# Optimization experiments

Hardware: AMD Instinct MI355X
Metric: run time of the kernel (lower is better)

Reference implementation:

```python
import jax, jax.numpy as jnp
import numpy as np

B, S, D, H = 4, 2048, 1024, 16
HD = D // H


def setup_inputs() -> dict:
    key = jax.random.key(0)
    ks = jax.random.split(key, 10)
    x = jax.random.normal(ks[0], (B, S, D), dtype=jnp.float32)
    mask = jnp.zeros((B, 1, 1, S), dtype=jnp.float32)  # 1 = masked, 0 = keep
    sc = 1.0 / np.sqrt(D)
    wq = jax.random.normal(ks[1], (D, D), dtype=jnp.float32) * sc
    wk = jax.random.normal(ks[2], (D, D), dtype=jnp.float32) * sc
    wv = jax.random.normal(ks[3], (D, D), dtype=jnp.float32) * sc
    wo = jax.random.normal(ks[4], (D, D), dtype=jnp.float32) * sc
    bq = jnp.zeros((D,), jnp.float32)
    bk = jnp.zeros((D,), jnp.float32)
    bv = jnp.zeros((D,), jnp.float32)
    bo = jnp.zeros((D,), jnp.float32)
    return {"x": x, "mask": mask, "wq": wq, "bq": bq, "wk": wk, "bk": bk,
            "wv": wv, "bv": bv, "wo": wo, "bo": bo}


def _split_heads(t):
    # (B, S, D) -> (B, H, S, HD)
    return t.reshape(B, -1, H, HD).transpose(0, 2, 1, 3)


def reference(x, mask, wq, bq, wk, bk, wv, bv, wo, bo):
    q = _split_heads(x @ wq + bq)
    k = _split_heads(x @ wk + bk)
    v = _split_heads(x @ wv + bv)
    # scaled dot-product attention (TF tutorial convention: mask*-1e9 added)
    scores = jnp.einsum("bhqd,bhkd->bhqk", q, k) / jnp.sqrt(jnp.float32(HD))
    scores = scores + mask * -1e9
    attn_weights = jax.nn.softmax(scores, axis=-1)  # (B, H, Sq, Sk)
    attn = jnp.einsum("bhqk,bhkd->bhqd", attn_weights, v)
    attn = attn.transpose(0, 2, 1, 3).reshape(B, -1, D)
    out = attn @ wo + bo
    return out, attn_weights
```

## Files before the change

### kernel.cpp

```cpp
#include <hip/hip_runtime.h>
#include <hip/hip_bf16.h>

#define S_LEN  2048
#define DMODEL 1024
#define NHEAD  16
#define HDIM   64
#define BSZ    4

#define C_SCORE  0.18033688f
#define C_MASK  -1.4426950e9f

typedef __bf16 bf16_t;
typedef __bf16 bf16x8 __attribute__((ext_vector_type(8)));
typedef __bf16 bf16x4 __attribute__((ext_vector_type(4)));
typedef float  f32x4  __attribute__((ext_vector_type(4)));

typedef __attribute__((address_space(1))) void as1_void;
typedef __attribute__((address_space(3))) void as3_void;

__device__ __forceinline__ f32x4 mfma16(bf16x8 a, bf16x8 b, f32x4 c) {
    return __builtin_amdgcn_mfma_f32_16x16x32_bf16(a, b, c, 0, 0, 0);
}

__global__ __launch_bounds__(256) void cvt_all(const float* __restrict__ x,
                                               bf16_t* __restrict__ xb,
                                               const float* __restrict__ w0,
                                               const float* __restrict__ w1,
                                               const float* __restrict__ w2,
                                               const float* __restrict__ w3,
                                               bf16_t* __restrict__ wT) {
    __shared__ bf16_t t[64][65];
    const int bid = blockIdx.x;
    if (bid < 4096) {
        const int i0 = bid * 256 + threadIdx.x;
        #pragma unroll
        for (int rep = 0; rep < 2; ++rep) {
            const int i = i0 + rep * 1048576;
            float4 v = ((const float4*)x)[i];
            bf16x4 tv = { (bf16_t)v.x, (bf16_t)v.y, (bf16_t)v.z, (bf16_t)v.w };
            ((bf16x4*)xb)[i] = tv;
        }
        return;
    }
    const int wb = bid - 4096;
    const int wsel = wb >> 8;
    const float* w = wsel == 0 ? w0 : (wsel == 1 ? w1 : (wsel == 2 ? w2 : w3));
    bf16_t* wTo = wT + (size_t)wsel * DMODEL * DMODEL;
    const int rb = wb & 255;
    const int bx = (rb & 15) * 64, by = (rb >> 4) * 64;
    const int tx = threadIdx.x & 63, ty = threadIdx.x >> 6;
    #pragma unroll
    for (int rr = 0; rr < 64; rr += 4)
        t[tx][rr + ty] = (bf16_t)w[(size_t)(bx + rr + ty) * DMODEL + by + tx];
    __syncthreads();
    #pragma unroll
    for (int rr = 0; rr < 64; rr += 4)
        wTo[(size_t)(by + rr + ty) * DMODEL + bx + tx] = t[rr + ty][tx];
}

template <int MODE>
__global__ __launch_bounds__(256) void gemm_bt(const bf16_t* __restrict__ A,
                                               const bf16_t* __restrict__ Bt,
                                               const float* __restrict__ b0,
                                               const float* __restrict__ b1,
                                               const float* __restrict__ b2,
                                               bf16_t* __restrict__ o0,
                                               bf16_t* __restrict__ o1,
                                               bf16_t* __restrict__ o2,
                                               float* __restrict__ of) {
    constexpr int GK = 1024;
    __shared__ __attribute__((aligned(16))) bf16_t smem_ab[8704];
    bf16_t* As = smem_ab;
    bf16_t* Bs = smem_ab + 4096;

    const int tid  = threadIdx.x;
    const int wave = tid >> 6, lane = tid & 63;
    const int col16 = lane & 15, g = lane >> 4;
    const int wr = wave >> 1, wc = wave & 1;
    const int bn0 = blockIdx.x * 128, bm0 = blockIdx.y * 128;

    const int r4 = tid >> 2;
    const int c8 = (tid & 3) * 8;

    f32x4 acc[4][4] = {};

    for (int k0 = 0; k0 < GK; k0 += 32) {
        __syncthreads();
        #pragma unroll
        for (int i = 0; i < 2; ++i) {
            __builtin_amdgcn_global_load_lds(
                (const as1_void*)(A + (size_t)(bm0 + i * 64 + r4) * GK + k0 + c8),
                (as3_void*)(As + (i * 64 + wave * 16) * 32), 16, 0, 0);
            __builtin_amdgcn_global_load_lds(
                (const as1_void*)(Bt + (size_t)(bn0 + i * 64 + r4) * GK + k0 + c8),
                (as3_void*)(Bs + (i * 64 + wave * 16) * 32), 16, 0, 0);
        }
        __syncthreads();

        bf16x8 af[4], bfr[4];
        #pragma unroll
        for (int i = 0; i < 4; ++i) {
            af[i]  = *(const bf16x8*)(As + (wr * 64 + i * 16 + col16) * 32 + g * 8);
            bfr[i] = *(const bf16x8*)(Bs + (wc * 64 + i * 16 + col16) * 32 + g * 8);
        }
        #pragma unroll
        for (int mi = 0; mi < 4; ++mi)
            #pragma unroll
            for (int ni = 0; ni < 4; ++ni)
                acc[mi][ni] = mfma16(af[mi], bfr[ni], acc[mi][ni]);
    }

    if (MODE == 0 && (bn0 >> 10) == 2) {
        const int n1base = bn0 - 2048;
        const int brow = bm0 >> 11;
        const int s0 = bm0 & 2047;
        __syncthreads();
        #pragma unroll
        for (int p = 0; p < 2; ++p) {
            if (p) __syncthreads();
            if (wc == p) {
                #pragma unroll
                for (int ni = 0; ni < 4; ++ni) {
                    const float bv = b2[n1base + p * 64 + ni * 16 + col16];
                    #pragma unroll
                    for (int mi = 0; mi < 4; ++mi) {
                        bf16x4 pv;
                        #pragma unroll
                        for (int r = 0; r < 4; ++r) pv[r] = (bf16_t)(acc[mi][ni][r] + bv);
                        *(bf16x4*)&smem_ab[(ni * 16 + col16) * 136 + wr * 64 + mi * 16 + g * 4] = pv;
                    }
                }
            }
            __syncthreads();
            const int h2 = (n1base + p * 64) >> 6;
            bf16_t* vout = o2 + (((size_t)brow * NHEAD + h2) * HDIM) * S_LEN + s0;
            #pragma unroll
            for (int j = 0; j < 4; ++j) {
                const int unit = j * 256 + tid;
                const int row = unit >> 4;
                const int cu = (unit & 15) * 8;
                bf16x8 v = *(const bf16x8*)&smem_ab[row * 136 + cu];
                *(bf16x8*)(vout + (size_t)row * S_LEN + cu) = v;
            }
        }
        return;
    }

    #pragma unroll
    for (int ni = 0; ni < 4; ++ni) {
        const int gn = bn0 + wc * 64 + ni * 16 + col16;
        if (MODE == 0) {
            const int proj = bn0 >> 10;
            const float* bias = proj == 0 ? b0 : b1;
            bf16_t* outp      = proj == 0 ? o0 : o1;
            const int n1 = gn & 1023, h = n1 >> 6, hd = n1 & 63;
            const float bv = bias[n1];
            #pragma unroll
            for (int mi = 0; mi < 4; ++mi)
                #pragma unroll
                for (int r = 0; r < 4; ++r) {
                    const int gm = bm0 + wr * 64 + mi * 16 + g * 4 + r;
                    const int b = gm >> 11, s = gm & 2047;
                    outp[(((size_t)b * NHEAD + h) * S_LEN + s) * HDIM + hd] =
                        (bf16_t)(acc[mi][ni][r] + bv);
                }
        } else {
            const float bv = b0[gn];
            #pragma unroll
            for (int mi = 0; mi < 4; ++mi)
                #pragma unroll
                for (int r = 0; r < 4; ++r) {
                    const int gm = bm0 + wr * 64 + mi * 16 + g * 4 + r;
                    of[(size_t)gm * DMODEL + gn] = acc[mi][ni][r] + bv;
                }
        }
    }
}

__global__ __launch_bounds__(512, 4) void attn_fused(const bf16_t* __restrict__ Q,
                                                     const bf16_t* __restrict__ K,
                                                     const bf16_t* __restrict__ Vt,
                                                     const float* __restrict__ mask,
                                                     float* __restrict__ attnW,
                                                     bf16_t* __restrict__ ctx) {
    __shared__ __attribute__((aligned(16))) char smem[73728];
    bf16_t (*KsA)[128][64] = (bf16_t(*)[128][64])smem;
    bf16_t (*Ks)[64][64]   = (bf16_t(*)[64][64])smem;
    bf16_t (*Vs)[64][64]   = (bf16_t(*)[64][64])(smem + 16384);
    float  (*Pl)[16][64]   = (float(*)[16][64])(smem + 32768);
    float*  Ml             = (float*)(smem + 65536);

    const int tid = threadIdx.x, wave = tid >> 6, lane = tid & 63;
    const int col16 = lane & 15, g = lane >> 4;
    const int r7 = col16 & 7;

    const int lin = blockIdx.x;
    const int logical = (lin & 7) * 64 + (lin >> 3);
    const int bh = logical >> 3, pp = logical & 7;
    const int b = bh >> 4, h = bh & 15;
    const int qA = pp * 256 + wave * 16;
    const int qB = pp * 256 + 128 + wave * 16;

    const bf16_t* Qb = Q + (size_t)bh * S_LEN * HDIM;
    const bf16_t* Kb = K + (size_t)bh * S_LEN * HDIM;
    const bf16_t* Vb = Vt + (size_t)bh * HDIM * S_LEN;
    const float* mp = mask + (size_t)b * S_LEN;

    {
        f32x4 v = ((const f32x4*)mp)[tid];
        #pragma unroll
        for (int r = 0; r < 4; ++r) v[r] *= C_MASK;
        *(f32x4*)(&Ml[tid * 4]) = v;
    }

    const int srow  = lane >> 3;
    const int sunit = (lane & 7) ^ srow;

    auto stageA = [&](int buf, int it) {
        const int kk0 = it << 7;
        #pragma unroll
        for (int i2 = 0; i2 < 2; ++i2) {
            const int i = wave * 2 + i2;
            __builtin_amdgcn_global_load_lds(
                (const as1_void*)(Kb + (size_t)(kk0 + i * 8 + srow) * HDIM + sunit * 8),
                (as3_void*)(&KsA[buf][i * 8][0]), 16, 0, 0);
        }
    };
    auto stageK = [&](int buf, int it) {
        const int kk0 = it << 6;
        __builtin_amdgcn_global_load_lds(
            (const as1_void*)(Kb + (size_t)(kk0 + wave * 8 + srow) * HDIM + sunit * 8),
            (as3_void*)(&Ks[buf][wave * 8][0]), 16, 0, 0);
    };
    auto stageV = [&](int buf, int it) {
        const int kk0 = it << 6;
        __builtin_amdgcn_global_load_lds(
            (const as1_void*)(Vb + (size_t)(wave * 8 + srow) * S_LEN + kk0 + sunit * 8),
            (as3_void*)(&Vs[buf][wave * 8][0]), 16, 0, 0);
    };
    auto kfrag = [&](int buf, int nj, int kh) {
        return *(const bf16x8*)(&Ks[buf][nj * 16 + col16][(((kh * 4 + g) ^ r7) * 8)]);
    };
    auto vfrag = [&](int buf, int nd, int kh) {
        return *(const bf16x8*)(&Vs[buf][nd * 16 + col16][(((kh * 4 + g) ^ r7) * 8)]);
    };

    bf16x8 qa0[2], qa1[2];
    #pragma unroll
    for (int kh = 0; kh < 2; ++kh) {
        qa0[kh] = *(const bf16x8*)(Qb + (size_t)(qA + col16) * HDIM + kh * 32 + g * 8);
        qa1[kh] = *(const bf16x8*)(Qb + (size_t)(qB + col16) * HDIM + kh * 32 + g * 8);
    }

    f32x4 lacc0 = {}, lacc1 = {};
    stageA(0, 0);
    __syncthreads();

    for (int it = 0; it < 16; ++it) {
        const int kk0 = it << 7, cur = it & 1;
        if (it < 15) stageA(cur ^ 1, it + 1);
        #pragma unroll
        for (int nj = 0; nj < 8; ++nj) {
            const f32x4 mvr = *(const f32x4*)(&Ml[kk0 + nj * 16 + g * 4]);
            const bf16x8 kf0 = *(const bf16x8*)(&KsA[cur][nj * 16 + col16][((g ^ r7) * 8)]);
            const bf16x8 kf1 = *(const bf16x8*)(&KsA[cur][nj * 16 + col16][(((4 + g) ^ r7) * 8)]);
            f32x4 t0 = {0.f, 0.f, 0.f, 0.f}, u0 = {0.f, 0.f, 0.f, 0.f};
            t0 = mfma16(kf0, qa0[0], t0);
            t0 = mfma16(kf1, qa0[1], t0);
            u0 = mfma16(kf0, qa1[0], u0);
            u0 = mfma16(kf1, qa1[1], u0);
            #pragma unroll
            for (int r = 0; r < 4; ++r) {
                lacc0[r] += exp2f(fmaf(t0[r], C_SCORE, mvr[r]));
                lacc1[r] += exp2f(fmaf(u0[r], C_SCORE, mvr[r]));
            }
        }
        asm volatile("s_waitcnt vmcnt(0)" ::: "memory");
        __builtin_amdgcn_sched_barrier(0);
        __builtin_amdgcn_s_barrier();
    }

    float crow0, crow1;
    {
        float lr0 = (lacc0[0] + lacc0[1]) + (lacc0[2] + lacc0[3]);
        lr0 += __shfl_xor(lr0, 16);
        lr0 += __shfl_xor(lr0, 32);
        crow0 = -__log2f(lr0);
        float lr1 = (lacc1[0] + lacc1[1]) + (lacc1[2] + lacc1[3]);
        lr1 += __shfl_xor(lr1, 16);
        lr1 += __shfl_xor(lr1, 32);
        crow1 = -__log2f(lr1);
    }

    f32x4 o0[4] = {}, o1[4] = {};
    float* awA = attnW + ((size_t)bh * S_LEN + qA) * S_LEN;
    float* awB = attnW + ((size_t)bh * S_LEN + qB) * S_LEN;

    stageK(0, 0);
    stageV(0, 0);
    asm volatile("s_waitcnt vmcnt(0)" ::: "memory");
    __builtin_amdgcn_sched_barrier(0);
    __builtin_amdgcn_s_barrier();

    for (int it = 0; it < 32; ++it) {
        const int kk0 = it << 6, cur = it & 1;
        if (it < 31) { stageK(cur ^ 1, it + 1); stageV(cur ^ 1, it + 1); }
        __builtin_amdgcn_sched_barrier(0);
        f32x4 mvr[4];
        #pragma unroll
        for (int nj = 0; nj < 4; ++nj)
            mvr[nj] = *(const f32x4*)(&Ml[kk0 + nj * 16 + g * 4]);

        #pragma unroll
        for (int nj = 0; nj < 4; ++nj) {
            const bf16x8 kf0 = kfrag(cur, nj, 0);
            const bf16x8 kf1 = kfrag(cur, nj, 1);
            f32x4 s0 = {0.f, 0.f, 0.f, 0.f};
            s0 = mfma16(kf0, qa0[0], s0);
            s0 = mfma16(kf1, qa0[1], s0);
            f32x4 pn0;
            #pragma unroll
            for (int r = 0; r < 4; ++r)
                pn0[r] = exp2f(fmaf(s0[r], C_SCORE, mvr[nj][r] + crow0));
            *(f32x4*)(&Pl[wave][col16][(((nj * 4 + g) ^ r7) * 4)]) = pn0;
        }
        #pragma unroll
        for (int j = 0; j < 4; ++j) {
            const int row = j * 4 + (lane >> 4);
            const int u = lane & 15;
            const f32x4 v = *(const f32x4*)(&Pl[wave][row][((u ^ (row & 7)) * 4)]);
            __builtin_nontemporal_store(v, (f32x4*)(awA + (size_t)row * S_LEN + kk0 + u * 4));
        }
        #pragma unroll
        for (int kh = 0; kh < 2; ++kh) {
            const int u0i = kh * 8 + g * 2;
            const f32x4 a0 = *(const f32x4*)(&Pl[wave][col16][((u0i ^ r7) * 4)]);
            const f32x4 a1 = *(const f32x4*)(&Pl[wave][col16][(((u0i + 1) ^ r7) * 4)]);
            bf16x8 pa;
            #pragma unroll
            for (int j = 0; j < 4; ++j) {
                pa[j]     = (bf16_t)a0[j];
                pa[4 + j] = (bf16_t)a1[j];
            }
            #pragma unroll
            for (int nd = 0; nd < 4; ++nd)
                o0[nd] = mfma16(vfrag(cur, nd, kh), pa, o0[nd]);
        }

        #pragma unroll
        for (int nj = 0; nj < 4; ++nj) {
            const bf16x8 kf0 = kfrag(cur, nj, 0);
            const bf16x8 kf1 = kfrag(cur, nj, 1);
            f32x4 s0 = {0.f, 0.f, 0.f, 0.f};
            s0 = mfma16(kf0, qa1[0], s0);
            s0 = mfma16(kf1, qa1[1], s0);
            f32x4 pn0;
            #pragma unroll
            for (int r = 0; r < 4; ++r)
                pn0[r] = exp2f(fmaf(s0[r], C_SCORE, mvr[nj][r] + crow1));
            *(f32x4*)(&Pl[wave][col16][(((nj * 4 + g) ^ r7) * 4)]) = pn0;
        }
        #pragma unroll
        for (int j = 0; j < 4; ++j) {
            const int row = j * 4 + (lane >> 4);
            const int u = lane & 15;
            const f32x4 v = *(const f32x4*)(&Pl[wave][row][((u ^ (row & 7)) * 4)]);
            __builtin_nontemporal_store(v, (f32x4*)(awB + (size_t)row * S_LEN + kk0 + u * 4));
        }
        #pragma unroll
        for (int kh = 0; kh < 2; ++kh) {
            const int u0i = kh * 8 + g * 2;
            const f32x4 a0 = *(const f32x4*)(&Pl[wave][col16][((u0i ^ r7) * 4)]);
            const f32x4 a1 = *(const f32x4*)(&Pl[wave][col16][(((u0i + 1) ^ r7) * 4)]);
            bf16x8 pa;
            #pragma unroll
            for (int j = 0; j < 4; ++j) {
                pa[j]     = (bf16_t)a0[j];
                pa[4 + j] = (bf16_t)a1[j];
            }
            #pragma unroll
            for (int nd = 0; nd < 4; ++nd)
                o1[nd] = mfma16(vfrag(cur, nd, kh), pa, o1[nd]);
        }

        asm volatile("s_waitcnt vmcnt(8)" ::: "memory");
        __builtin_amdgcn_sched_barrier(0);
        __builtin_amdgcn_s_barrier();
    }

    {
        bf16_t* cpA = ctx + ((size_t)b * S_LEN + qA + col16) * DMODEL + h * HDIM;
        bf16_t* cpB = ctx + ((size_t)b * S_LEN + qB + col16) * DMODEL + h * HDIM;
        #pragma unroll
        for (int nd = 0; nd < 4; ++nd) {
            bf16x4 cv0, cv1;
            #pragma unroll
            for (int r = 0; r < 4; ++r) {
                cv0[r] = (bf16_t)o0[nd][r];
                cv1[r] = (bf16_t)o1[nd][r];
            }
            *(bf16x4*)(cpA + nd * 16 + g * 4) = cv0;
            *(bf16x4*)(cpB + nd * 16 + g * 4) = cv1;
        }
    }
}

extern "C" void kernel_launch(void* const* d_in, const int* in_sizes, int n_in,
                              void* d_out, int out_size, void* d_ws, size_t ws_size,
                              hipStream_t stream) {
    const float* x    = (const float*)d_in[0];
    const float* mask = (const float*)d_in[1];
    const float* wq   = (const float*)d_in[2];
    const float* bq   = (const float*)d_in[3];
    const float* wk   = (const float*)d_in[4];
    const float* bk   = (const float*)d_in[5];
    const float* wv   = (const float*)d_in[6];
    const float* bv   = (const float*)d_in[7];
    const float* wo   = (const float*)d_in[8];
    const float* bo   = (const float*)d_in[9];

    const size_t nX = (size_t)BSZ * S_LEN * DMODEL;
    const size_t nW = (size_t)DMODEL * DMODEL;

    char* ws = (char*)d_ws;
    size_t off = 0;
    bf16_t* xb     = (bf16_t*)(ws + off); off += nX * 2;
    bf16_t* wqkvT  = (bf16_t*)(ws + off); off += 3 * nW * 2;
    bf16_t* woT    = (bf16_t*)(ws + off); off += nW * 2;
    bf16_t* qbh    = (bf16_t*)(ws + off); off += nX * 2;
    bf16_t* kbh    = (bf16_t*)(ws + off); off += nX * 2;
    bf16_t* vtb    = (bf16_t*)(ws + off); off += nX * 2;
    bf16_t* ctx    = (bf16_t*)(ws + off); off += nX * 2;
    if (ws_size < off) return;

    float* outp  = (float*)d_out;
    float* attnW = outp + nX;

    cvt_all<<<5120, 256, 0, stream>>>(x, xb, wq, wk, wv, wo, wqkvT);

    gemm_bt<0><<<dim3(24, 64), 256, 0, stream>>>(xb, wqkvT, bq, bk, bv,
                                                 qbh, kbh, vtb, nullptr);

    attn_fused<<<512, 512, 0, stream>>>(qbh, kbh, vtb, mask, attnW, ctx);

    gemm_bt<2><<<dim3(8, 64), 256, 0, stream>>>(ctx, woT, bo, nullptr, nullptr,
                                                nullptr, nullptr, nullptr, outp);
}
```

Before: 369.0 us.

## Triple-buffer K/V staging and halve the per-wave P scratch tile

Moves the K/V (and first-pass K) shared-memory staging from double to triple buffering, prefetching two tiles ahead with vmcnt waits tuned to leave outstanding loads in flight. The freed LDS comes from shrinking the per-wave probability scratch from 64 to 32 columns, so each 64-key tile is now processed in two halves for the store and the PV MFMA. The goal is to hide global-load latency behind compute. The risks are fragile hand-counted vmcnt values that must match the actual load and store counts, more LDS round trips, and extra modulo-3 indexing.

```diff
diff --git a/kernel.cpp b/kernel.cpp
--- a/kernel.cpp
+++ b/kernel.cpp
@@ -186,8 +186,8 @@
     __shared__ __attribute__((aligned(16))) char smem[73728];
     bf16_t (*KsA)[128][64] = (bf16_t(*)[128][64])smem;
     bf16_t (*Ks)[64][64]   = (bf16_t(*)[64][64])smem;
-    bf16_t (*Vs)[64][64]   = (bf16_t(*)[64][64])(smem + 16384);
-    float  (*Pl)[16][64]   = (float(*)[16][64])(smem + 32768);
+    bf16_t (*Vs)[64][64]   = (bf16_t(*)[64][64])(smem + 24576);
+    float  (*Pl)[16][32]   = (float(*)[16][32])(smem + 49152);
     float*  Ml             = (float*)(smem + 65536);
 
     const int tid = threadIdx.x, wave = tid >> 6, lane = tid & 63;
@@ -254,11 +254,12 @@
 
     f32x4 lacc0 = {}, lacc1 = {};
     stageA(0, 0);
+    stageA(1, 1);
     __syncthreads();
 
     for (int it = 0; it < 16; ++it) {
-        const int kk0 = it << 7, cur = it & 1;
-        if (it < 15) stageA(cur ^ 1, it + 1);
+        const int kk0 = it << 7, cur = it % 3;
+        if (it < 14) stageA((it + 2) % 3, it + 2);
         #pragma unroll
         for (int nj = 0; nj < 8; ++nj) {
             const f32x4 mvr = *(const f32x4*)(&Ml[kk0 + nj * 16 + g * 4]);
@@ -275,7 +276,8 @@
                 lacc1[r] += exp2f(fmaf(u0[r], C_SCORE, mvr[r]));
             }
         }
-        asm volatile("s_waitcnt vmcnt(0)" ::: "memory");
+        if (it < 14) { asm volatile("s_waitcnt vmcnt(2)" ::: "memory"); }
+        else         { asm volatile("s_waitcnt vmcnt(0)" ::: "memory"); }
         __builtin_amdgcn_sched_barrier(0);
         __builtin_amdgcn_s_barrier();
     }
@@ -298,13 +300,19 @@
 
     stageK(0, 0);
     stageV(0, 0);
-    asm volatile("s_waitcnt vmcnt(0)" ::: "memory");
+    stageK(1, 1);
+    stageV(1, 1);
+    asm volatile("s_waitcnt vmcnt(2)" ::: "memory");
     __builtin_amdgcn_sched_barrier(0);
     __builtin_amdgcn_s_barrier();
 
     for (int it = 0; it < 32; ++it) {
-        const int kk0 = it << 6, cur = it & 1;
-        if (it < 31) { stageK(cur ^ 1, it + 1); stageV(cur ^ 1, it + 1); }
+        const int kk0 = it << 6, cur = it % 3;
+        if (it < 30) {
+            const int nb = (it + 2) % 3;
+            stageK(nb, it + 2);
+            stageV(nb, it + 2);
+        }
         __builtin_amdgcn_sched_barrier(0);
         f32x4 mvr[4];
         #pragma unroll
@@ -312,78 +320,86 @@
             mvr[nj] = *(const f32x4*)(&Ml[kk0 + nj * 16 + g * 4]);
 
         #pragma unroll
-        for (int nj = 0; nj < 4; ++nj) {
-            const bf16x8 kf0 = kfrag(cur, nj, 0);
-            const bf16x8 kf1 = kfrag(cur, nj, 1);
-            f32x4 s0 = {0.f, 0.f, 0.f, 0.f};
-            s0 = mfma16(kf0, qa0[0], s0);
-            s0 = mfma16(kf1, qa0[1], s0);
-            f32x4 pn0;
-            #pragma unroll
-            for (int r = 0; r < 4; ++r)
-                pn0[r] = exp2f(fmaf(s0[r], C_SCORE, mvr[nj][r] + crow0));
-            *(f32x4*)(&Pl[wave][col16][(((nj * 4 + g) ^ r7) * 4)]) = pn0;
-        }
-        #pragma unroll
-        for (int j = 0; j < 4; ++j) {
-            const int row = j * 4 + (lane >> 4);
-            const int u = lane & 15;
-            const f32x4 v = *(const f32x4*)(&Pl[wave][row][((u ^ (row & 7)) * 4)]);
-            __builtin_nontemporal_store(v, (f32x4*)(awA + (size_t)row * S_LEN + kk0 + u * 4));
-        }
-        #pragma unroll
-        for (int kh = 0; kh < 2; ++kh) {
-            const int u0i = kh * 8 + g * 2;
-            const f32x4 a0 = *(const f32x4*)(&Pl[wave][col16][((u0i ^ r7) * 4)]);
-            const f32x4 a1 = *(const f32x4*)(&Pl[wave][col16][(((u0i + 1) ^ r7) * 4)]);
-            bf16x8 pa;
-            #pragma unroll
-            for (int j = 0; j < 4; ++j) {
-                pa[j]     = (bf16_t)a0[j];
-                pa[4 + j] = (bf16_t)a1[j];
-            }
-            #pragma unroll
-            for (int nd = 0; nd < 4; ++nd)
-                o0[nd] = mfma16(vfrag(cur, nd, kh), pa, o0[nd]);
-        }
-
-        #pragma unroll
-        for (int nj = 0; nj < 4; ++nj) {
-            const bf16x8 kf0 = kfrag(cur, nj, 0);
-            const bf16x8 kf1 = kfrag(cur, nj, 1);
-            f32x4 s0 = {0.f, 0.f, 0.f, 0.f};
-            s0 = mfma16(kf0, qa1[0], s0);
-            s0 = mfma16(kf1, qa1[1], s0);
-            f32x4 pn0;
-            #pragma unroll
-            for (int r = 0; r < 4; ++r)
-                pn0[r] = exp2f(fmaf(s0[r], C_SCORE, mvr[nj][r] + crow1));
-            *(f32x4*)(&Pl[wave][col16][(((nj * 4 + g) ^ r7) * 4)]) = pn0;
-        }
-        #pragma unroll
-        for (int j = 0; j < 4; ++j) {
-            const int row = j * 4 + (lane >> 4);
-            const int u = lane & 15;
-            const f32x4 v = *(const f32x4*)(&Pl[wave][row][((u ^ (row & 7)) * 4)]);
-            __builtin_nontemporal_store(v, (f32x4*)(awB + (size_t)row * S_LEN + kk0 + u * 4));
-        }
-        #pragma unroll
-        for (int kh = 0; kh < 2; ++kh) {
-            const int u0i = kh * 8 + g * 2;
-            const f32x4 a0 = *(const f32x4*)(&Pl[wave][col16][((u0i ^ r7) * 4)]);
-            const f32x4 a1 = *(const f32x4*)(&Pl[wave][col16][(((u0i + 1) ^ r7) * 4)]);
-            bf16x8 pa;
-            #pragma unroll
-            for (int j = 0; j < 4; ++j) {
-                pa[j]     = (bf16_t)a0[j];
-                pa[4 + j] = (bf16_t)a1[j];
-            }
-            #pragma unroll
-            for (int nd = 0; nd < 4; ++nd)
-                o1[nd] = mfma16(vfrag(cur, nd, kh), pa, o1[nd]);
-        }
-
-        asm volatile("s_waitcnt vmcnt(8)" ::: "memory");
+        for (int hf = 0; hf < 2; ++hf) {
+            #pragma unroll
+            for (int nj2 = 0; nj2 < 2; ++nj2) {
+                const int nj = hf * 2 + nj2;
+                const bf16x8 kf0 = kfrag(cur, nj, 0);
+                const bf16x8 kf1 = kfrag(cur, nj, 1);
+                f32x4 s0 = {0.f, 0.f, 0.f, 0.f};
+                s0 = mfma16(kf0, qa0[0], s0);
+                s0 = mfma16(kf1, qa0[1], s0);
+                f32x4 pn;
+                #pragma unroll
+                for (int r = 0; r < 4; ++r)
+                    pn[r] = exp2f(fmaf(s0[r], C_SCORE, mvr[nj][r] + crow0));
+                *(f32x4*)(&Pl[wave][col16][(((nj2 * 4 + g) ^ r7) * 4)]) = pn;
+            }
+            #pragma unroll
+            for (int j = 0; j < 2; ++j) {
+                const int row = j * 8 + (lane >> 3);
+                const int u = lane & 7;
+                const f32x4 v = *(const f32x4*)(&Pl[wave][row][((u ^ (row & 7)) * 4)]);
+                __builtin_nontemporal_store(v,
+                    (f32x4*)(awA + (size_t)row * S_LEN + kk0 + hf * 32 + u * 4));
+            }
+            {
+                const f32x4 a0 = *(const f32x4*)(&Pl[wave][col16][(((2 * g) ^ r7) * 4)]);
+                const f32x4 a1 = *(const f32x4*)(&Pl[wave][col16][(((2 * g + 1) ^ r7) * 4)]);
+                bf16x8 pa;
+                #pragma unroll
+                for (int j = 0; j < 4; ++j) {
+                    pa[j]     = (bf16_t)a0[j];
+                    pa[4 + j] = (bf16_t)a1[j];
+                }
+                #pragma unroll
+                for (int nd = 0; nd < 4; ++nd)
+                    o0[nd] = mfma16(vfrag(cur, nd, hf), pa, o0[nd]);
+            }
+        }
+
+        #pragma unroll
+        for (int hf = 0; hf < 2; ++hf) {
+            #pragma unroll
+            for (int nj2 = 0; nj2 < 2; ++nj2) {
+                const int nj = hf * 2 + nj2;
+                const bf16x8 kf0 = kfrag(cur, nj, 0);
+                const bf16x8 kf1 = kfrag(cur, nj, 1);
+                f32x4 s0 = {0.f, 0.f, 0.f, 0.f};
+                s0 = mfma16(kf0, qa1[0], s0);
+                s0 = mfma16(kf1, qa1[1], s0);
+                f32x4 pn;
+                #pragma unroll
+                for (int r = 0; r < 4; ++r)
+                    pn[r] = exp2f(fmaf(s0[r], C_SCORE, mvr[nj][r] + crow1));
+                *(f32x4*)(&Pl[wave][col16][(((nj2 * 4 + g) ^ r7) * 4)]) = pn;
+            }
+            #pragma unroll
+            for (int j = 0; j < 2; ++j) {
+                const int row = j * 8 + (lane >> 3);
+                const int u = lane & 7;
+                const f32x4 v = *(const f32x4*)(&Pl[wave][row][((u ^ (row & 7)) * 4)]);
+                __builtin_nontemporal_store(v,
+                    (f32x4*)(awB + (size_t)row * S_LEN + kk0 + hf * 32 + u * 4));
+            }
+            {
+                const f32x4 a0 = *(const f32x4*)(&Pl[wave][col16][(((2 * g) ^ r7) * 4)]);
+                const f32x4 a1 = *(const f32x4*)(&Pl[wave][col16][(((2 * g + 1) ^ r7) * 4)]);
+                bf16x8 pa;
+                #pragma unroll
+                for (int j = 0; j < 4; ++j) {
+                    pa[j]     = (bf16_t)a0[j];
+                    pa[4 + j] = (bf16_t)a1[j];
+                }
+                #pragma unroll
+                for (int nd = 0; nd < 4; ++nd)
+                    o1[nd] = mfma16(vfrag(cur, nd, hf), pa, o1[nd]);
+            }
+        }
+
+        if (it == 0)      { asm volatile("s_waitcnt vmcnt(10)" ::: "memory"); }
+        else if (it < 30) { asm volatile("s_waitcnt vmcnt(18)" ::: "memory"); }
+        else              { asm volatile("s_waitcnt vmcnt(16)" ::: "memory"); }
         __builtin_amdgcn_sched_barrier(0);
         __builtin_amdgcn_s_barrier();
     }
```

Result: slower. 384.4 us (+4.2%).
